# Kernel optimization log

Hardware: AMD Instinct MI355X
Metric: run time of the kernel (lower is better)

Reference implementation:

```python
import jax, jax.numpy as jnp
import numpy as np

N_NODES = 50000
N_EDGES = 800000
D = 128


def _gcn_norm(edge_index, edge_weights, n_nodes):
    # PyG gcn_norm with add_self_loops=True, fill_value=1.0
    src = jnp.concatenate([edge_index[0], jnp.arange(n_nodes)])
    dst = jnp.concatenate([edge_index[1], jnp.arange(n_nodes)])
    w = jnp.concatenate([edge_weights, jnp.ones((n_nodes,), edge_weights.dtype)])
    deg = jax.ops.segment_sum(w, dst, num_segments=n_nodes)
    dinv = jnp.where(deg > 0, jax.lax.rsqrt(deg), 0.0)
    norm = dinv[src] * w * dinv[dst]  # [E + N]
    return src, dst, norm


def _gcn_conv(x, src, dst, norm, W, b, n_nodes):
    h = x @ W                                   # [N, F_out]
    msg = h[src] * norm[:, None]                # gather + scale, [E+N, F_out]
    out = jax.ops.segment_sum(msg, dst, num_segments=n_nodes)
    return out + b


def setup_inputs() -> dict:
    key = jax.random.key(0)
    ks = jax.random.split(key, 12)
    s = 1.0 / np.sqrt(D)
    return {
        "x": jax.random.normal(ks[0], (N_NODES, D), jnp.float32),
        "edge_index": jax.random.randint(ks[1], (2, N_EDGES), 0, N_NODES, jnp.int64),
        "edge_weights": jax.random.uniform(ks[2], (N_EDGES,), jnp.float32),
        "W1": jax.random.normal(ks[3], (D, D), jnp.float32) * s,
        "b1": jnp.zeros((D,), jnp.float32),
        "W2": jax.random.normal(ks[4], (D, D), jnp.float32) * s,
        "b2": jnp.zeros((D,), jnp.float32),
        "W3": jax.random.normal(ks[5], (D, D), jnp.float32) * s,
        "b3": jnp.zeros((D,), jnp.float32),
        "Wl": jax.random.normal(ks[6], (D, D), jnp.float32) * s,
        "bl": jnp.zeros((D,), jnp.float32),
    }


def reference(x, edge_index, edge_weights, W1, b1, W2, b2, W3, b3, Wl, bl):
    n = x.shape[0]
    src, dst, norm = _gcn_norm(edge_index, edge_weights, n)
    h = _gcn_conv(x, src, dst, norm, W1, b1, n)
    h = jax.nn.relu(h)
    h = _gcn_conv(h, src, dst, norm, W2, b2, n)
    h = jax.nn.relu(h)
    h = _gcn_conv(h, src, dst, norm, W3, b3, n)
    # final 'linear' activation entry == nn.Linear(out_size, out_size)
    return h @ Wl + bl
```

## Files before the change

kernel.cpp:

```cpp
#include <hip/hip_runtime.h>
#include <hip/hip_fp16.h>


#define D 128
#define CNT64_STRIDE 8
#define SLOTS 64

typedef __attribute__((ext_vector_type(8))) _Float16 half8;
typedef __attribute__((ext_vector_type(4))) float floatx4;

template <bool A_IS_F32>
__device__ __forceinline__ void gemm_body(int bid, const void* Aptr,
                                          const float* W, const float* bias,
                                          float* C32, __half* C16, int N) {
    __shared__ _Float16 Wl[128][136];
    int tid = threadIdx.x;

#pragma unroll
    for (int j = 0; j < 32; j++) {
        int e = tid + j * 512;
        Wl[e & 127][e >> 7] = (_Float16)W[e];
    }
    __syncthreads();

    int wave = tid >> 6, lane = tid & 63;
    int m = lane & 15, q = lane >> 4;
    int R0 = bid * 128 + wave * 16;

    const float*  A32p = (const float*)Aptr;
    const __half* A16p = (const __half*)Aptr;

    floatx4 acc[8];
#pragma unroll
    for (int ct = 0; ct < 8; ct++) acc[ct] = (floatx4){0.f, 0.f, 0.f, 0.f};

    int arow = R0 + m;
    bool rok = arow < N;

#pragma unroll
    for (int kk = 0; kk < 4; kk++) {
        half8 a = {0, 0, 0, 0, 0, 0, 0, 0};
        if (rok) {
            if (A_IS_F32) {
                const float* p = &A32p[(size_t)arow * 128 + kk * 32 + q * 8];
                float4 f0 = *(const float4*)p;
                float4 f1 = *(const float4*)(p + 4);
                a[0] = (_Float16)f0.x; a[1] = (_Float16)f0.y;
                a[2] = (_Float16)f0.z; a[3] = (_Float16)f0.w;
                a[4] = (_Float16)f1.x; a[5] = (_Float16)f1.y;
                a[6] = (_Float16)f1.z; a[7] = (_Float16)f1.w;
            } else {
                a = *(const half8*)&A16p[(size_t)arow * 128 + kk * 32 + q * 8];
            }
        }
#pragma unroll
        for (int ct = 0; ct < 8; ct++) {
            half8 b = *(const half8*)&Wl[ct * 16 + m][kk * 32 + q * 8];
            acc[ct] = __builtin_amdgcn_mfma_f32_16x16x32_f16(a, b, acc[ct], 0, 0, 0);
        }
    }

#pragma unroll
    for (int r = 0; r < 4; r++) {
        int row = R0 + q * 4 + r;
        if (row >= N) continue;
#pragma unroll
        for (int ct = 0; ct < 8; ct++) {
            int col = ct * 16 + m;
            float v = acc[ct][r];
            if (C16) C16[(size_t)row * 128 + col] = __float2half_rn(v);
            if (C32) C32[(size_t)row * 128 + col] = v + bias[col];
        }
    }
}

template <bool A_IS_F32>
__global__ __launch_bounds__(512) void k_gemm_mfma(const void* __restrict__ Aptr,
                                                   const float* __restrict__ W,
                                                   const float* __restrict__ bias,
                                                   float* __restrict__ C32,
                                                   __half* __restrict__ C16, int N) {
    gemm_body<A_IS_F32>(blockIdx.x, Aptr, W, bias, C32, C16, N);
}

__global__ __launch_bounds__(512) void k_build_gemm1(const float* __restrict__ x,
                                                     const float* __restrict__ W1,
                                                     __half* __restrict__ y16,
                                                     const int* __restrict__ dst,
                                                     const float* __restrict__ w,
                                                     unsigned long long* __restrict__ cnt8,
                                                     int* __restrict__ loc,
                                                     int N, int E, int gg, int ggp) {
    int b = (int)blockIdx.x;
    if (b < gg) {
        gemm_body<true>(b, x, W1, nullptr, nullptr, y16, N);
        return;
    }
    if (b < ggp) return;
    int e = (b - ggp) * 512 + threadIdx.x;
    if (e < E) {
        int d = dst[e];
        unsigned int wq = __float2uint_rn(w[e] * 32767.0f);
        unsigned long long old =
            atomicAdd(&cnt8[(size_t)d * CNT64_STRIDE], (1ull << 32) | (unsigned long long)wq);
        loc[e] = (int)(old >> 32);
    }
}

__global__ __launch_bounds__(256) void k_fill(const int* __restrict__ ei,
                                              const float* __restrict__ w,
                                              const unsigned int* __restrict__ wsum32,
                                              const int* __restrict__ loc,
                                              unsigned int* __restrict__ ev, int E) {
    int e = blockIdx.x * 256 + threadIdx.x;
    if (e < E) {
        int s = ei[e];
        int d = ei[E + e];
        float dvs = rsqrtf(1.0f + (float)wsum32[(size_t)s * 16] * (1.0f / 32767.0f));
        float dvd = rsqrtf(1.0f + (float)wsum32[(size_t)d * 16] * (1.0f / 32767.0f));
        float val = w[e] * dvs * dvd;
        unsigned int wq = __float2uint_rn(val * 32767.0f);
        ev[(size_t)d * SLOTS + loc[e]] = (wq << 17) | (unsigned int)s;
    }
}

__device__ __forceinline__ void fma8(float acc[8], float v, uint4 q) {
    union { uint4 uu; __half h[8]; } U; U.uu = q;
#pragma unroll
    for (int j = 0; j < 8; j++)
        acc[j] = fmaf(__half2float(U.h[j]), v, acc[j]);
}

__global__ __launch_bounds__(256) void k_agg(const __half* __restrict__ y16,
                                             const unsigned long long* __restrict__ cnt8,
                                             const unsigned int* __restrict__ ev,
                                             const float* __restrict__ bias,
                                             __half* __restrict__ out16,
                                             int N, int relu) {
    int wave = threadIdx.x >> 6;
    int lane = threadIdx.x & 63;
    int h  = lane >> 5;
    int r5 = lane & 31;
    int g  = r5 >> 4;
    int sl = r5 & 15;

    int i = blockIdx.x * 8 + wave * 2 + h;
    if (i >= N) return;

    const unsigned int* evp = ev + (size_t)i * SLOTS;

    unsigned long long pk = cnt8[(size_t)i * CNT64_STRIDE];
    uint4 ea = *(const uint4*)&evp[g * 8];
    uint4 eb = *(const uint4*)&evp[g * 8 + 4];
    uint4 selfq = make_uint4(0, 0, 0, 0);
    float4 b0 = make_float4(0.f, 0.f, 0.f, 0.f);
    float4 b1 = make_float4(0.f, 0.f, 0.f, 0.f);
    if (g == 0) {
        selfq = *(const uint4*)&y16[(size_t)i * D + sl * 8];
        b0 = *(const float4*)&bias[sl * 8];
        b1 = *(const float4*)&bias[sl * 8 + 4];
    }

    int cnt = min((int)(pk >> 32), SLOTS);
    float di = rsqrtf(1.0f + (float)(unsigned int)pk * (1.0f / 32767.0f));

    float acc[8];
#pragma unroll
    for (int j = 0; j < 8; j++) acc[j] = 0.f;

    {
        unsigned int p[8] = {ea.x, ea.y, ea.z, ea.w, eb.x, eb.y, eb.z, eb.w};
        float v[8]; uint4 q4[8];
#pragma unroll
        for (int u = 0; u < 8; u++) {
            bool ok = (g * 8 + u) < cnt;
            v[u] = ok ? (float)(p[u] >> 17) * (1.0f / 32767.0f) : 0.0f;
            int s = min((int)(p[u] & 0x1FFFFu), N - 1);
            q4[u] = *(const uint4*)&y16[(size_t)s * D + sl * 8];
        }
#pragma unroll
        for (int u = 0; u < 8; u++) fma8(acc, v[u], q4[u]);
    }

    for (int base = 16; base < cnt; base += 16) {
        uint4 ta = *(const uint4*)&evp[base + g * 8];
        uint4 tb = *(const uint4*)&evp[base + g * 8 + 4];
        unsigned int p[8] = {ta.x, ta.y, ta.z, ta.w, tb.x, tb.y, tb.z, tb.w};
        float v[8]; uint4 q4[8];
#pragma unroll
        for (int u = 0; u < 8; u++) {
            bool ok = (base + g * 8 + u) < cnt;
            v[u] = ok ? (float)(p[u] >> 17) * (1.0f / 32767.0f) : 0.0f;
            int s = min((int)(p[u] & 0x1FFFFu), N - 1);
            q4[u] = *(const uint4*)&y16[(size_t)s * D + sl * 8];
        }
#pragma unroll
        for (int u = 0; u < 8; u++) fma8(acc, v[u], q4[u]);
    }

#pragma unroll
    for (int j = 0; j < 8; j++) acc[j] += __shfl_xor(acc[j], 16, 64);

    if (g == 0) {
        float di2 = di * di;
        union { uint4 u; __half h[8]; } S; S.u = selfq;
        float o[8];
        o[0] = b0.x + acc[0] + di2 * __half2float(S.h[0]);
        o[1] = b0.y + acc[1] + di2 * __half2float(S.h[1]);
        o[2] = b0.z + acc[2] + di2 * __half2float(S.h[2]);
        o[3] = b0.w + acc[3] + di2 * __half2float(S.h[3]);
        o[4] = b1.x + acc[4] + di2 * __half2float(S.h[4]);
        o[5] = b1.y + acc[5] + di2 * __half2float(S.h[5]);
        o[6] = b1.z + acc[6] + di2 * __half2float(S.h[6]);
        o[7] = b1.w + acc[7] + di2 * __half2float(S.h[7]);
        if (relu) {
#pragma unroll
            for (int j = 0; j < 8; j++) o[j] = fmaxf(o[j], 0.f);
        }
        union { uint4 u; __half2 h2[4]; } O;
        O.h2[0] = __float22half2_rn(make_float2(o[0], o[1]));
        O.h2[1] = __float22half2_rn(make_float2(o[2], o[3]));
        O.h2[2] = __float22half2_rn(make_float2(o[4], o[5]));
        O.h2[3] = __float22half2_rn(make_float2(o[6], o[7]));
        *(uint4*)&out16[(size_t)i * D + sl * 8] = O.u;
    }
}

extern "C" void kernel_launch(void* const* d_in, const int* in_sizes, int n_in,
                              void* d_out, int out_size, void* d_ws, size_t ws_size,
                              hipStream_t stream) {
    const float* x  = (const float*)d_in[0];
    const int*   ei = (const int*)d_in[1];
    const float* ew = (const float*)d_in[2];
    const float* W1 = (const float*)d_in[3];
    const float* b1 = (const float*)d_in[4];
    const float* W2 = (const float*)d_in[5];
    const float* b2 = (const float*)d_in[6];
    const float* W3 = (const float*)d_in[7];
    const float* b3 = (const float*)d_in[8];
    const float* Wl = (const float*)d_in[9];
    const float* bl = (const float*)d_in[10];

    int N = in_sizes[0] / D;
    int E = in_sizes[2];

    char* ws = (char*)d_ws;
    size_t off = 0;
    auto alloc = [&](size_t bytes) {
        void* p = ws + off;
        off = (off + bytes + 255) & ~(size_t)255;
        return p;
    };
    unsigned long long* cnt8 = (unsigned long long*)alloc((size_t)N * 64);
    int*    loc  = (int*)alloc((size_t)E * 4);
    unsigned int* ev = (unsigned int*)alloc((size_t)N * SLOTS * 4);
    __half* yA   = (__half*)alloc((size_t)N * D * 2);
    __half* yB   = (__half*)alloc((size_t)N * D * 2);

    int nbE    = (E + 255) / 256;
    int nbE512 = (E + 511) / 512;
    int gg     = (N + 127) / 128;
    int ggp    = (gg + 7) & ~7;
    int ga     = (N + 7) / 8;

    hipMemsetAsync(cnt8, 0, (size_t)N * 64, stream);
    k_build_gemm1<<<ggp + nbE512, 512, 0, stream>>>(x, W1, yA, ei + E, ew,
                                                    cnt8, loc, N, E, gg, ggp);
    k_fill<<<nbE, 256, 0, stream>>>(ei, ew, (const unsigned int*)cnt8, loc, ev, E);

    k_agg<<<ga, 256, 0, stream>>>(yA, cnt8, ev, b1, yB, N, 1);
    k_gemm_mfma<false><<<gg, 512, 0, stream>>>(yB, W2, nullptr, nullptr, yA, N);
    k_agg<<<ga, 256, 0, stream>>>(yA, cnt8, ev, b2, yB, N, 1);
    k_gemm_mfma<false><<<gg, 512, 0, stream>>>(yB, W3, nullptr, nullptr, yA, N);
    k_agg<<<ga, 256, 0, stream>>>(yA, cnt8, ev, b3, yB, N, 0);
    k_gemm_mfma<false><<<gg, 512, 0, stream>>>(yB, Wl, bl, (float*)d_out, nullptr, N);
}
```

Baseline: 277.8 us.

## Fuse whole GCN pipeline into one cooperative persistent kernel with grid syncs

Replaces the sequence of nine launches (memset, build+gemm1, fill, three agg and three gemm kernels) with a single cooperative kernel that loops over tiles persistently and separates phases with grid-wide syncs. The aim is to remove launch gaps and tail effects between the many short kernels. In exchange, each grid.sync costs time, occupancy is capped by the 512-thread block with a large shared W tile, and the first-layer gemm restages W1 for every tile. The original multi-kernel path remains as a fallback when cooperative launch fails.

```diff
diff --git a/kernel.cpp b/kernel.cpp
--- a/kernel.cpp
+++ b/kernel.cpp
@@ -1,5 +1,8 @@
 #include <hip/hip_runtime.h>
 #include <hip/hip_fp16.h>
+#include <hip/hip_cooperative_groups.h>
+
+namespace cg = cooperative_groups;
 
 
 #define D 128
@@ -9,20 +12,23 @@
 typedef __attribute__((ext_vector_type(8))) _Float16 half8;
 typedef __attribute__((ext_vector_type(4))) float floatx4;
 
-template <bool A_IS_F32>
-__device__ __forceinline__ void gemm_body(int bid, const void* Aptr,
-                                          const float* W, const float* bias,
-                                          float* C32, __half* C16, int N) {
-    __shared__ _Float16 Wl[128][136];
+
+__device__ __forceinline__ void stage_W(const float* __restrict__ W,
+                                        _Float16 (*Wl)[136]) {
     int tid = threadIdx.x;
-
 #pragma unroll
     for (int j = 0; j < 32; j++) {
         int e = tid + j * 512;
         Wl[e & 127][e >> 7] = (_Float16)W[e];
     }
-    __syncthreads();
-
+}
+
+template <bool A_IS_F32>
+__device__ __forceinline__ void gemm_tile(int bid, const void* Aptr,
+                                          const float* bias, float* C32,
+                                          __half* C16, int N,
+                                          const _Float16 (*Wl)[136]) {
+    int tid = threadIdx.x;
     int wave = tid >> 6, lane = tid & 63;
     int m = lane & 15, q = lane >> 4;
     int R0 = bid * 128 + wave * 16;
@@ -74,30 +80,10 @@
     }
 }
 
-template <bool A_IS_F32>
-__global__ __launch_bounds__(512) void k_gemm_mfma(const void* __restrict__ Aptr,
-                                                   const float* __restrict__ W,
-                                                   const float* __restrict__ bias,
-                                                   float* __restrict__ C32,
-                                                   __half* __restrict__ C16, int N) {
-    gemm_body<A_IS_F32>(blockIdx.x, Aptr, W, bias, C32, C16, N);
-}
-
-__global__ __launch_bounds__(512) void k_build_gemm1(const float* __restrict__ x,
-                                                     const float* __restrict__ W1,
-                                                     __half* __restrict__ y16,
-                                                     const int* __restrict__ dst,
-                                                     const float* __restrict__ w,
-                                                     unsigned long long* __restrict__ cnt8,
-                                                     int* __restrict__ loc,
-                                                     int N, int E, int gg, int ggp) {
-    int b = (int)blockIdx.x;
-    if (b < gg) {
-        gemm_body<true>(b, x, W1, nullptr, nullptr, y16, N);
-        return;
-    }
-    if (b < ggp) return;
-    int e = (b - ggp) * 512 + threadIdx.x;
+__device__ __forceinline__ void edge_work(int e, const int* __restrict__ dst,
+                                          const float* __restrict__ w,
+                                          unsigned long long* __restrict__ cnt8,
+                                          int* __restrict__ loc, int E) {
     if (e < E) {
         int d = dst[e];
         unsigned int wq = __float2uint_rn(w[e] * 32767.0f);
@@ -107,12 +93,11 @@
     }
 }
 
-__global__ __launch_bounds__(256) void k_fill(const int* __restrict__ ei,
-                                              const float* __restrict__ w,
-                                              const unsigned int* __restrict__ wsum32,
-                                              const int* __restrict__ loc,
-                                              unsigned int* __restrict__ ev, int E) {
-    int e = blockIdx.x * 256 + threadIdx.x;
+__device__ __forceinline__ void fill_work(int e, const int* __restrict__ ei,
+                                          const float* __restrict__ w,
+                                          const unsigned int* __restrict__ wsum32,
+                                          const int* __restrict__ loc,
+                                          unsigned int* __restrict__ ev, int E) {
     if (e < E) {
         int s = ei[e];
         int d = ei[E + e];
@@ -131,22 +116,13 @@
         acc[j] = fmaf(__half2float(U.h[j]), v, acc[j]);
 }
 
-__global__ __launch_bounds__(256) void k_agg(const __half* __restrict__ y16,
-                                             const unsigned long long* __restrict__ cnt8,
-                                             const unsigned int* __restrict__ ev,
-                                             const float* __restrict__ bias,
-                                             __half* __restrict__ out16,
-                                             int N, int relu) {
-    int wave = threadIdx.x >> 6;
-    int lane = threadIdx.x & 63;
-    int h  = lane >> 5;
-    int r5 = lane & 31;
-    int g  = r5 >> 4;
-    int sl = r5 & 15;
-
-    int i = blockIdx.x * 8 + wave * 2 + h;
-    if (i >= N) return;
-
+__device__ __forceinline__ void agg_node(int i, int g, int sl,
+                                         const __half* __restrict__ y16,
+                                         const unsigned long long* __restrict__ cnt8,
+                                         const unsigned int* __restrict__ ev,
+                                         const float* __restrict__ bias,
+                                         __half* __restrict__ out16,
+                                         int N, int relu) {
     const unsigned int* evp = ev + (size_t)i * SLOTS;
 
     unsigned long long pk = cnt8[(size_t)i * CNT64_STRIDE];
@@ -224,6 +200,145 @@
         O.h2[3] = __float22half2_rn(make_float2(o[6], o[7]));
         *(uint4*)&out16[(size_t)i * D + sl * 8] = O.u;
     }
+}
+
+
+__device__ __forceinline__ void gemm_sweep(const void* A, const float* W,
+                                           const float* bias, float* C32,
+                                           __half* C16, int N, int gg, int gsz,
+                                           _Float16 (*Wl)[136]) {
+    stage_W(W, Wl);
+    __syncthreads();
+    for (int t = blockIdx.x; t < gg; t += gsz)
+        gemm_tile<false>(t, A, bias, C32, C16, N, Wl);
+    __syncthreads();
+}
+
+__device__ __forceinline__ void agg_sweep(const __half* y, const unsigned long long* cnt8,
+                                          const unsigned int* ev, const float* bias,
+                                          __half* out, int N, int relu, int gsz) {
+    int wave = threadIdx.x >> 6;
+    int lane = threadIdx.x & 63;
+    int h  = lane >> 5;
+    int r5 = lane & 31;
+    int g  = r5 >> 4;
+    int sl = r5 & 15;
+    int nv = (N + 15) / 16;
+    for (int c = blockIdx.x; c < nv; c += gsz) {
+        int i = c * 16 + wave * 2 + h;
+        if (i < N) agg_node(i, g, sl, y, cnt8, ev, bias, out, N, relu);
+    }
+}
+
+__global__ __launch_bounds__(512) void k_all(
+    const float* __restrict__ x, const int* __restrict__ ei,
+    const float* __restrict__ ew,
+    const float* __restrict__ W1, const float* __restrict__ b1,
+    const float* __restrict__ W2, const float* __restrict__ b2,
+    const float* __restrict__ W3, const float* __restrict__ b3,
+    const float* __restrict__ Wlw, const float* __restrict__ bl,
+    unsigned long long* __restrict__ cnt8, int* __restrict__ loc,
+    unsigned int* __restrict__ ev, __half* __restrict__ yA,
+    __half* __restrict__ yB, float* __restrict__ outp, int N, int E) {
+    __shared__ _Float16 Wl[128][136];
+    cg::grid_group grid = cg::this_grid();
+    const int gsz = gridDim.x;
+    const int tid = threadIdx.x;
+    const int gg = (N + 127) >> 7;
+    const int ne = (E + 511) >> 9;
+
+    {
+        int total = N * 4;
+        for (int t = blockIdx.x * 512 + tid; t < total; t += gsz * 512)
+            ((uint4*)cnt8)[t] = make_uint4(0, 0, 0, 0);
+    }
+    __threadfence(); grid.sync();
+
+    for (int vb = blockIdx.x; vb < gg + ne; vb += gsz) {
+        if (vb < gg) {
+            stage_W(W1, Wl);
+            __syncthreads();
+            gemm_tile<true>(vb, x, nullptr, nullptr, yA, N, Wl);
+            __syncthreads();
+        } else {
+            edge_work((vb - gg) * 512 + tid, ei + E, ew, cnt8, loc, E);
+        }
+    }
+    __threadfence(); grid.sync();
+
+    for (int vb = blockIdx.x; vb < ne; vb += gsz)
+        fill_work(vb * 512 + tid, ei, ew, (const unsigned int*)cnt8, loc, ev, E);
+    __threadfence(); grid.sync();
+
+    agg_sweep(yA, cnt8, ev, b1, yB, N, 1, gsz);
+    __threadfence(); grid.sync();
+    gemm_sweep(yB, W2, nullptr, nullptr, yA, N, gg, gsz, Wl);
+    __threadfence(); grid.sync();
+    agg_sweep(yA, cnt8, ev, b2, yB, N, 1, gsz);
+    __threadfence(); grid.sync();
+    gemm_sweep(yB, W3, nullptr, nullptr, yA, N, gg, gsz, Wl);
+    __threadfence(); grid.sync();
+    agg_sweep(yA, cnt8, ev, b3, yB, N, 0, gsz);
+    __threadfence(); grid.sync();
+    gemm_sweep(yB, Wlw, bl, outp, nullptr, N, gg, gsz, Wl);
+}
+
+
+template <bool A_IS_F32>
+__global__ __launch_bounds__(512) void k_gemm_mfma(const void* __restrict__ Aptr,
+                                                   const float* __restrict__ W,
+                                                   const float* __restrict__ bias,
+                                                   float* __restrict__ C32,
+                                                   __half* __restrict__ C16, int N) {
+    __shared__ _Float16 Wl[128][136];
+    stage_W(W, Wl);
+    __syncthreads();
+    gemm_tile<A_IS_F32>(blockIdx.x, Aptr, bias, C32, C16, N, Wl);
+}
+
+__global__ __launch_bounds__(512) void k_build_gemm1(const float* __restrict__ x,
+                                                     const float* __restrict__ W1,
+                                                     __half* __restrict__ y16,
+                                                     const int* __restrict__ dst,
+                                                     const float* __restrict__ w,
+                                                     unsigned long long* __restrict__ cnt8,
+                                                     int* __restrict__ loc,
+                                                     int N, int E, int gg, int ggp) {
+    int b = (int)blockIdx.x;
+    if (b < gg) {
+        __shared__ _Float16 Wl[128][136];
+        stage_W(W1, Wl);
+        __syncthreads();
+        gemm_tile<true>(b, x, nullptr, nullptr, y16, N, Wl);
+        return;
+    }
+    if (b < ggp) return;
+    edge_work((b - ggp) * 512 + threadIdx.x, dst, w, cnt8, loc, E);
+}
+
+__global__ __launch_bounds__(256) void k_fill(const int* __restrict__ ei,
+                                              const float* __restrict__ w,
+                                              const unsigned int* __restrict__ wsum32,
+                                              const int* __restrict__ loc,
+                                              unsigned int* __restrict__ ev, int E) {
+    fill_work(blockIdx.x * 256 + threadIdx.x, ei, w, wsum32, loc, ev, E);
+}
+
+__global__ __launch_bounds__(256) void k_agg(const __half* __restrict__ y16,
+                                             const unsigned long long* __restrict__ cnt8,
+                                             const unsigned int* __restrict__ ev,
+                                             const float* __restrict__ bias,
+                                             __half* __restrict__ out16,
+                                             int N, int relu) {
+    int wave = threadIdx.x >> 6;
+    int lane = threadIdx.x & 63;
+    int h  = lane >> 5;
+    int r5 = lane & 31;
+    int g  = r5 >> 4;
+    int sl = r5 & 15;
+    int i = blockIdx.x * 8 + wave * 2 + h;
+    if (i >= N) return;
+    agg_node(i, g, sl, y16, cnt8, ev, bias, out16, N, relu);
 }
 
 extern "C" void kernel_launch(void* const* d_in, const int* in_sizes, int n_in,
@@ -256,6 +371,30 @@
     unsigned int* ev = (unsigned int*)alloc((size_t)N * SLOTS * 4);
     __half* yA   = (__half*)alloc((size_t)N * D * 2);
     __half* yB   = (__half*)alloc((size_t)N * D * 2);
+    float*  outp = (float*)d_out;
+
+    bool done = false;
+    int dev = 0, coop = 0;
+    (void)hipGetDevice(&dev);
+    (void)hipDeviceGetAttribute(&coop, hipDeviceAttributeCooperativeLaunch, dev);
+    if (coop) {
+        int maxb = 0;
+        (void)hipOccupancyMaxActiveBlocksPerMultiprocessor(&maxb, k_all, 512, 0);
+        if (maxb > 0) {
+            int G = maxb * 256;
+            if (G > 2048) G = 2048;
+            void* args[] = {(void*)&x,  (void*)&ei, (void*)&ew,
+                            (void*)&W1, (void*)&b1, (void*)&W2, (void*)&b2,
+                            (void*)&W3, (void*)&b3, (void*)&Wl, (void*)&bl,
+                            (void*)&cnt8, (void*)&loc, (void*)&ev,
+                            (void*)&yA, (void*)&yB, (void*)&outp,
+                            (void*)&N, (void*)&E};
+            hipError_t err = hipLaunchCooperativeKernel(
+                k_all, dim3(G), dim3(512), args, 0, stream);
+            done = (err == hipSuccess);
+        }
+    }
+    if (done) return;
 
     int nbE    = (E + 255) / 256;
     int nbE512 = (E + 511) / 512;
@@ -263,7 +402,7 @@
     int ggp    = (gg + 7) & ~7;
     int ga     = (N + 7) / 8;
 
-    hipMemsetAsync(cnt8, 0, (size_t)N * 64, stream);
+    (void)hipMemsetAsync(cnt8, 0, (size_t)N * 64, stream);
     k_build_gemm1<<<ggp + nbE512, 512, 0, stream>>>(x, W1, yA, ei + E, ew,
                                                     cnt8, loc, N, E, gg, ggp);
     k_fill<<<nbE, 256, 0, stream>>>(ei, ew, (const unsigned int*)cnt8, loc, ev, E);
@@ -273,5 +412,5 @@
     k_agg<<<ga, 256, 0, stream>>>(yA, cnt8, ev, b2, yB, N, 1);
     k_gemm_mfma<false><<<gg, 512, 0, stream>>>(yB, W3, nullptr, nullptr, yA, N);
     k_agg<<<ga, 256, 0, stream>>>(yA, cnt8, ev, b3, yB, N, 0);
-    k_gemm_mfma<false><<<gg, 512, 0, stream>>>(yB, Wl, bl, (float*)d_out, nullptr, N);
-}
+    k_gemm_mfma<false><<<gg, 512, 0, stream>>>(yB, Wl, bl, outp, nullptr, N);
+}
```

Result: no change. 279.5 us (+0.6%).
